# Optimization experiments

Hardware: AMD Instinct MI355X
Metric: run time of the kernel (lower is better)

Reference implementation:

```python
import jax, jax.numpy as jnp
import numpy as np

N = 100000   # nodes
E = 1600000  # edges
IN = 32      # input_dim == num_concepts
H = 128      # h_dim == num_concepts * dim_per_concept
C = 32       # num_concepts
D = 4        # dim_per_concept
G = 32       # g_dim of per-concept MLPs
LAMBDAV = 1e-3


def _spmm(edge_src, edge_dst, edge_val, x):
    # sparse adjacency matmul: out[d] = sum_{edges e: dst(e)=d} val(e) * x[src(e)]
    return jax.ops.segment_sum(edge_val[:, None] * x[edge_src], edge_dst, num_segments=N)


def setup_inputs() -> dict:
    key = jax.random.key(0)
    ks = jax.random.split(key, 20)
    s = lambda shape: 1.0 / np.sqrt(shape[-1] if len(shape) > 1 else 1)
    inp = {
        'X': jax.random.normal(ks[0], (N, IN), jnp.float32),
        'label': jax.random.uniform(ks[1], (N, C), jnp.float32),
        'edge_val': jax.random.uniform(ks[2], (E,), jnp.float32),
        'noise': jax.random.normal(ks[3], (N, C, D), jnp.float32),
        'W_base': jax.random.normal(ks[4], (IN, H), jnp.float32) / np.sqrt(IN),
        'W_mean': jax.random.normal(ks[5], (H, H), jnp.float32) / np.sqrt(H),
        'W_logstd': jax.random.normal(ks[6], (H, H), jnp.float32) / np.sqrt(H),
        'A': 0.05 * jax.random.normal(ks[7], (C, C), jnp.float32),  # keep I - A^T well-conditioned
        'Wz1': jax.random.normal(ks[8], (C, D, G), jnp.float32) / np.sqrt(D),
        'bz1': jax.random.normal(ks[9], (C, G), jnp.float32) * 0.01,
        'Wz2': jax.random.normal(ks[10], (C, G, D), jnp.float32) / np.sqrt(G),
        'bz2': jax.random.normal(ks[11], (C, D), jnp.float32) * 0.01,
        'Wl1': jax.random.normal(ks[12], (C, 1, G), jnp.float32),
        'bl1': jax.random.normal(ks[13], (C, G), jnp.float32) * 0.01,
        'Wl2': jax.random.normal(ks[14], (C, G, 1), jnp.float32) / np.sqrt(G),
        'bl2': jax.random.normal(ks[15], (C, 1), jnp.float32) * 0.01,
        'Wrec': jax.random.normal(ks[16], (H, IN), jnp.float32) / np.sqrt(H),
        'brec': jax.random.normal(ks[17], (IN,), jnp.float32) * 0.01,
        'edge_src': jax.random.randint(ks[18], (E,), 0, N),
        'edge_dst': jax.random.randint(ks[19], (E,), 0, N),
    }
    return inp


def reference(X, label, edge_val, noise, W_base, W_mean, W_logstd, A,
              Wz1, bz1, Wz2, bz2, Wl1, bl1, Wl2, bl2, Wrec, brec,
              edge_src, edge_dst):
    # ---- sparse GCN encoder (x branch): GraphConvSparse = act(spmm(adj, x @ W)) ----
    hidden = jax.nn.relu(_spmm(edge_src, edge_dst, edge_val, X @ W_base))   # [N, H]
    e_m = _spmm(edge_src, edge_dst, edge_val, hidden @ W_mean)              # [N, H]
    _ = _spmm(edge_src, edge_dst, edge_val, hidden @ W_logstd)              # computed then discarded (e_v := ones) in source
    e_m = e_m.reshape(N, C, D)                                              # [N, C, D]

    # ---- CausalDAG: z = (I - A^T)^{-1} epsilon along the concept axis ----
    I = jnp.eye(C, dtype=X.dtype)
    Cmat = jnp.linalg.inv(I - A.T)                                          # [C, C]
    z_m = jnp.einsum('ck,nkd->ncd', Cmat, e_m)                              # [N, C, D]

    # mask: A^T @ x along concept axis
    masked_z_m = jnp.einsum('ck,nkd->ncd', A.T, z_m)                        # [N, C, D]
    masked_label = jnp.einsum('ck,nk->nc', A.T, label)[..., None]           # [N, C, 1]

    # g_z: per-concept MLP Linear(D,G)-ELU-Linear(G,D), weights stacked over concepts
    hz = jax.nn.elu(jnp.einsum('ncd,cdg->ncg', masked_z_m, Wz1) + bz1[None])
    masked_z_m = jnp.einsum('ncg,cgd->ncd', hz, Wz2) + bz2[None]            # [N, C, D]

    # g_label: per-concept MLP Linear(1,G)-ELU-Linear(G,1)
    hl = jax.nn.elu(jnp.einsum('nce,ceg->ncg', masked_label, Wl1) + bl1[None])
    pred_label = (jnp.einsum('ncg,cge->nce', hl, Wl2) + bl2[None])[..., 0]  # [N, C]

    # conditional_sample_gaussian with v = e_v * lambdav, e_v = ones
    z = masked_z_m + jnp.sqrt(jnp.asarray(LAMBDAV, X.dtype)) * noise        # [N, C, D]

    # pred_x / reconst_X head
    rec_x = z.reshape(N, H) @ Wrec + brec                                   # [N, IN]
    return rec_x, pred_label
```

## Files before the change

kernel.cpp:

```cpp
#include <hip/hip_runtime.h>
#include <hip/hip_bf16.h>

#define N_NODES 100000
#define N_EDGES 1600000
#define NBUCK   391
#define EHIST_G 196

static __device__ __forceinline__ float us2f(unsigned short u) {
    union { unsigned int i; float f; } cv; cv.i = ((unsigned int)u) << 16; return cv.f;
}
static __device__ __forceinline__ unsigned short f2us(float f) {
    __hip_bfloat16 b = __float2bfloat16(f);
    union { __hip_bfloat16 b; unsigned short u; } cv; cv.b = b; return cv.u;
}
static __device__ __forceinline__ float elu_fast(float v) {
    return v > 0.f ? v : (__expf(v) - 1.0f);
}

__global__ __launch_bounds__(64) void k_inv(const float* __restrict__ A,
                                            float* __restrict__ MmT) {
    __shared__ float Af[1024];
    __shared__ float aug[32 * 65];
    __shared__ float fac[32];
    __shared__ float pv_s;
    int t = threadIdx.x;
    for (int i = t; i < 1024; i += 64) Af[i] = A[i];
    __syncthreads();
    for (int i = t; i < 2048; i += 64) {
        int r = i >> 6, c = i & 63;
        float v;
        if (c < 32) v = (r == c ? 1.0f : 0.0f) - Af[c * 32 + r];
        else        v = ((c - 32) == r ? 1.0f : 0.0f);
        aug[r * 65 + c] = v;
    }
    __syncthreads();
    for (int k = 0; k < 32; ++k) {
        if (t == 0) pv_s = 1.0f / aug[k * 65 + k];
        __syncthreads();
        aug[k * 65 + t] *= pv_s;
        __syncthreads();
        if (t < 32) fac[t] = aug[t * 65 + k];
        __syncthreads();
        #pragma unroll 4
        for (int i = t; i < 2048; i += 64) {
            int r = i >> 6, c = i & 63;
            if (r != k) aug[r * 65 + c] -= fac[r] * aug[k * 65 + c];
        }
        __syncthreads();
    }
    for (int i = t; i < 1024; i += 64) {
        int j = i >> 5, c = i & 31;
        float s = 0.f;
        #pragma unroll
        for (int k = 0; k < 32; ++k) s += Af[k * 32 + c] * aug[k * 65 + 32 + j];
        MmT[i] = s;
    }
}

__global__ __launch_bounds__(256) void k_fold(const float* __restrict__ MmT,
                                              const float* __restrict__ Wm,
                                              float* __restrict__ Wcomb) {
    __shared__ float MmTs[1024];
    int tid = threadIdx.x;
    for (int i = tid; i < 1024; i += 256) MmTs[i] = MmT[i];
    __syncthreads();
    int o = blockIdx.x * 256 + tid;
    int h = o >> 5, c = o & 31;
    float4 s = {0.f, 0.f, 0.f, 0.f};
    #pragma unroll
    for (int j = 0; j < 32; ++j) {
        float m = MmTs[j * 32 + c];
        float4 w = ((const float4*)Wm)[h * 32 + j];
        s.x += m * w.x; s.y += m * w.y; s.z += m * w.z; s.w += m * w.w;
    }
    ((float4*)Wcomb)[o] = s;
}

__global__ __launch_bounds__(256) void k_bhist(const int* __restrict__ edst,
                                               unsigned int* __restrict__ bucket_deg) {
    __shared__ unsigned int h[NBUCK];
    int tid = threadIdx.x;
    int e0 = blockIdx.x * 8192;
    for (int i = tid; i < NBUCK; i += 256) h[i] = 0u;
    __syncthreads();
    #pragma unroll 4
    for (int k = 0; k < 32; ++k) {
        int e = e0 + k * 256 + tid;
        if (e < N_EDGES) atomicAdd(&h[((unsigned)edst[e]) >> 8], 1u);
    }
    __syncthreads();
    for (int b = tid; b < NBUCK; b += 256) {
        unsigned int v = h[b];
        if (v) atomicAdd(&bucket_deg[b], v);
    }
}

__global__ __launch_bounds__(512) void k_bscan(const unsigned int* __restrict__ bucket_deg,
                                               unsigned int* __restrict__ bucket_start,
                                               unsigned int* __restrict__ bucket_cursor) {
    __shared__ unsigned int s[512];
    int tid = threadIdx.x;
    unsigned int v = (tid < NBUCK) ? bucket_deg[tid] : 0u;
    s[tid] = v;
    __syncthreads();
    for (int off = 1; off < 512; off <<= 1) {
        unsigned int x = (tid >= off) ? s[tid - off] : 0u;
        __syncthreads();
        s[tid] += x;
        __syncthreads();
    }
    if (tid < NBUCK) {
        unsigned int excl = s[tid] - v;
        bucket_start[tid] = excl;
        bucket_cursor[tid] = excl;
    }
    if (tid == 0) bucket_start[NBUCK] = N_EDGES;
}

__global__ __launch_bounds__(256) void k_bucket1(const int* __restrict__ esrc,
                                                 const int* __restrict__ edst,
                                                 const float* __restrict__ evalv,
                                                 unsigned int* __restrict__ bucket_cursor,
                                                 uint2* __restrict__ coarse,
                                                 unsigned char* __restrict__ coarse_dl) {
    __shared__ unsigned int hist[NBUCK];
    __shared__ unsigned int gbase[NBUCK];
    __shared__ unsigned int lcnt[NBUCK];
    int tid = threadIdx.x;
    int e0 = blockIdx.x * 8192;
    for (int i = tid; i < NBUCK; i += 256) { hist[i] = 0u; lcnt[i] = 0u; }
    __syncthreads();
    #pragma unroll 4
    for (int k = 0; k < 32; ++k) {
        int e = e0 + k * 256 + tid;
        if (e < N_EDGES) atomicAdd(&hist[((unsigned)edst[e]) >> 8], 1u);
    }
    __syncthreads();
    for (int b = tid; b < NBUCK; b += 256) {
        unsigned int h = hist[b];
        gbase[b] = h ? atomicAdd(&bucket_cursor[b], h) : 0u;
    }
    __syncthreads();
    #pragma unroll 4
    for (int k = 0; k < 32; ++k) {
        int e = e0 + k * 256 + tid;
        if (e < N_EDGES) {
            unsigned int d = (unsigned)edst[e];
            unsigned int b = d >> 8;
            unsigned int r = atomicAdd(&lcnt[b], 1u);
            unsigned int p = gbase[b] + r;
            uint2 ev;
            ev.x = (unsigned int)esrc[e];
            ev.y = __float_as_uint(evalv[e]);
            coarse[p] = ev;
            coarse_dl[p] = (unsigned char)(d & 255u);
        }
    }
}

__global__ __launch_bounds__(256) void k_bucket2(const unsigned int* __restrict__ bucket_start,
                                                 const uint2* __restrict__ coarse,
                                                 const unsigned char* __restrict__ coarse_dl,
                                                 unsigned int* __restrict__ row_start,
                                                 uint2* __restrict__ edge_sorted) {
    __shared__ unsigned int h[256];
    __shared__ unsigned int sc[256];
    int b = blockIdx.x;
    int tid = threadIdx.x;
    unsigned int bs = bucket_start[b];
    unsigned int be = bucket_start[b + 1];
    h[tid] = 0u;
    __syncthreads();
    for (unsigned int i = bs + tid; i < be; i += 256)
        atomicAdd(&h[coarse_dl[i]], 1u);
    __syncthreads();
    unsigned int v = h[tid];
    sc[tid] = v;
    __syncthreads();
    for (int off = 1; off < 256; off <<= 1) {
        unsigned int x = (tid >= off) ? sc[tid - off] : 0u;
        __syncthreads();
        sc[tid] += x;
        __syncthreads();
    }
    unsigned int excl = sc[tid] - v;
    int node = (b << 8) + tid;
    if (node < N_NODES) row_start[node] = bs + excl;
    if (b == 0 && tid == 0) row_start[N_NODES] = N_EDGES;
    h[tid] = excl;
    __syncthreads();
    for (unsigned int i = bs + tid; i < be; i += 256) {
        uint2 ev = coarse[i];
        unsigned int dl = coarse_dl[i];
        unsigned int r = atomicAdd(&h[dl], 1u);
        edge_sorted[bs + r] = ev;
    }
}

__global__ __launch_bounds__(256) void k_fuse1(const unsigned int* __restrict__ row_start,
                                               const uint2* __restrict__ edge_sorted,
                                               const float* __restrict__ X,
                                               const float* __restrict__ Wb,
                                               unsigned short* __restrict__ hidden) {
    __shared__ float Wb_s[4096];
    __shared__ float s1r[8 * 33];
    int tid = threadIdx.x;
    for (int i = tid; i < 1024; i += 256)
        ((float4*)Wb_s)[i] = ((const float4*)Wb)[i];

    int lane = tid & 31;
    int nd = tid >> 5;
    int n = blockIdx.x * 8 + nd;
    unsigned int i = row_start[n], e = row_start[n + 1];
    float a0 = 0.f, a1 = 0.f, a2 = 0.f, a3 = 0.f;
    for (; i + 4 <= e; i += 4) {
        uint2 ea = edge_sorted[i + 0], eb = edge_sorted[i + 1];
        uint2 ec = edge_sorted[i + 2], ed = edge_sorted[i + 3];
        float xa = X[(size_t)ea.x * 32 + lane];
        float xb = X[(size_t)eb.x * 32 + lane];
        float xc = X[(size_t)ec.x * 32 + lane];
        float xd = X[(size_t)ed.x * 32 + lane];
        a0 += __uint_as_float(ea.y) * xa;
        a1 += __uint_as_float(eb.y) * xb;
        a2 += __uint_as_float(ec.y) * xc;
        a3 += __uint_as_float(ed.y) * xd;
    }
    for (; i < e; ++i) {
        uint2 ea = edge_sorted[i];
        a0 += __uint_as_float(ea.y) * X[(size_t)ea.x * 32 + lane];
    }
    s1r[nd * 33 + lane] = (a0 + a1) + (a2 + a3);
    __syncthreads();

    int q = lane * 4;
    float4 acc = {0.f, 0.f, 0.f, 0.f};
    #pragma unroll
    for (int k = 0; k < 32; ++k) {
        float v = s1r[nd * 33 + k];
        float4 w = *(const float4*)&Wb_s[k * 128 + q];
        acc.x += v * w.x; acc.y += v * w.y; acc.z += v * w.z; acc.w += v * w.w;
    }
    ushort4 o;
    o.x = f2us(fmaxf(acc.x, 0.f)); o.y = f2us(fmaxf(acc.y, 0.f));
    o.z = f2us(fmaxf(acc.z, 0.f)); o.w = f2us(fmaxf(acc.w, 0.f));
    *(ushort4*)&hidden[(size_t)n * 128 + q] = o;
}

__global__ __launch_bounds__(256) void k_gather2(const unsigned int* __restrict__ row_start,
                                                 const uint2* __restrict__ edge_sorted,
                                                 const unsigned short* __restrict__ hidden,
                                                 unsigned short* __restrict__ S2) {
    int lane = threadIdx.x & 31;
    int n = blockIdx.x * 8 + (threadIdx.x >> 5);
    unsigned int i = row_start[n], e = row_start[n + 1];
    float4 A0 = {0, 0, 0, 0}, A1 = {0, 0, 0, 0}, A2 = {0, 0, 0, 0}, A3 = {0, 0, 0, 0};
    for (; i + 4 <= e; i += 4) {
        uint2 ea = edge_sorted[i + 0], eb = edge_sorted[i + 1];
        uint2 ec = edge_sorted[i + 2], ed = edge_sorted[i + 3];
        ushort4 ha = *(const ushort4*)&hidden[(size_t)ea.x * 128 + lane * 4];
        ushort4 hb = *(const ushort4*)&hidden[(size_t)eb.x * 128 + lane * 4];
        ushort4 hc = *(const ushort4*)&hidden[(size_t)ec.x * 128 + lane * 4];
        ushort4 hd = *(const ushort4*)&hidden[(size_t)ed.x * 128 + lane * 4];
        float va = __uint_as_float(ea.y), vb = __uint_as_float(eb.y);
        float vc = __uint_as_float(ec.y), vd = __uint_as_float(ed.y);
        A0.x += va * us2f(ha.x); A0.y += va * us2f(ha.y); A0.z += va * us2f(ha.z); A0.w += va * us2f(ha.w);
        A1.x += vb * us2f(hb.x); A1.y += vb * us2f(hb.y); A1.z += vb * us2f(hb.z); A1.w += vb * us2f(hb.w);
        A2.x += vc * us2f(hc.x); A2.y += vc * us2f(hc.y); A2.z += vc * us2f(hc.z); A2.w += vc * us2f(hc.w);
        A3.x += vd * us2f(hd.x); A3.y += vd * us2f(hd.y); A3.z += vd * us2f(hd.z); A3.w += vd * us2f(hd.w);
    }
    for (; i < e; ++i) {
        uint2 ea = edge_sorted[i];
        float v = __uint_as_float(ea.y);
        ushort4 h = *(const ushort4*)&hidden[(size_t)ea.x * 128 + lane * 4];
        A0.x += v * us2f(h.x); A0.y += v * us2f(h.y); A0.z += v * us2f(h.z); A0.w += v * us2f(h.w);
    }
    float4 acc;
    acc.x = (A0.x + A1.x) + (A2.x + A3.x);
    acc.y = (A0.y + A1.y) + (A2.y + A3.y);
    acc.z = (A0.z + A1.z) + (A2.z + A3.z);
    acc.w = (A0.w + A1.w) + (A2.w + A3.w);
    ushort4 o;
    o.x = f2us(acc.x); o.y = f2us(acc.y); o.z = f2us(acc.z); o.w = f2us(acc.w);
    *(ushort4*)&S2[(size_t)n * 128 + lane * 4] = o;
}

__global__ __launch_bounds__(256) void k_gemm2(const unsigned short* __restrict__ S2,
                                               const float* __restrict__ Wc,
                                               unsigned short* __restrict__ mt4) {
    __shared__ float Wc_s[128 * 64];
    __shared__ float S2s[32 * 132];
    __shared__ unsigned short Tt[64 * 40];
    int tid = threadIdx.x;
    int rb = blockIdx.x >> 1;
    int j0 = (blockIdx.x & 1) * 64;
    int n0 = rb * 32;
    for (int idx = tid; idx < 2048; idx += 256) {
        int k = idx >> 4, jq = idx & 15;
        *(float4*)&Wc_s[k * 64 + jq * 4] = *(const float4*)&Wc[k * 128 + j0 + jq * 4];
    }
    for (int idx = tid; idx < 1024; idx += 256) {
        int r = idx >> 5, kq = idx & 31;
        ushort4 h = *(const ushort4*)&S2[(size_t)(n0 + r) * 128 + kq * 4];
        float4 f = {us2f(h.x), us2f(h.y), us2f(h.z), us2f(h.w)};
        *(float4*)&S2s[r * 132 + kq * 4] = f;
    }
    __syncthreads();
    int q = (tid & 15) * 4;
    int r0 = tid >> 4;
    float4 a0 = {0, 0, 0, 0}, a1 = {0, 0, 0, 0};
    for (int k4 = 0; k4 < 128; k4 += 4) {
        float4 s0 = *(const float4*)&S2s[r0 * 132 + k4];
        float4 s1 = *(const float4*)&S2s[(r0 + 16) * 132 + k4];
        #pragma unroll
        for (int kk = 0; kk < 4; ++kk) {
            float v0 = (&s0.x)[kk];
            float v1 = (&s1.x)[kk];
            float4 w = *(const float4*)&Wc_s[(k4 + kk) * 64 + q];
            a0.x += v0 * w.x; a0.y += v0 * w.y; a0.z += v0 * w.z; a0.w += v0 * w.w;
            a1.x += v1 * w.x; a1.y += v1 * w.y; a1.z += v1 * w.z; a1.w += v1 * w.w;
        }
    }
    #pragma unroll
    for (int c = 0; c < 4; ++c) {
        Tt[(q + c) * 40 + r0]      = f2us((&a0.x)[c]);
        Tt[(q + c) * 40 + r0 + 16] = f2us((&a1.x)[c]);
    }
    __syncthreads();
    int cc = tid >> 4;
    int r  = (tid & 15) * 2;
    int cg = (j0 >> 2) + cc;
    #pragma unroll
    for (int rr = 0; rr < 2; ++rr) {
        ushort4 o;
        o.x = Tt[(cc * 4 + 0) * 40 + r + rr];
        o.y = Tt[(cc * 4 + 1) * 40 + r + rr];
        o.z = Tt[(cc * 4 + 2) * 40 + r + rr];
        o.w = Tt[(cc * 4 + 3) * 40 + r + rr];
        *(ushort4*)&mt4[((size_t)cg * N_NODES + n0 + r + rr) * 4] = o;
    }
}

__global__ __launch_bounds__(256) void k_noisew(const float* __restrict__ noise,
                                                const float* __restrict__ Wrec,
                                                const float* __restrict__ brec,
                                                float* __restrict__ noiseW) {
    __shared__ float Wr[4096];
    __shared__ float Ns[64 * 132];
    __shared__ float brs[32];
    int tid = threadIdx.x;
    int n0 = blockIdx.x * 64;
    const float SQ = 0.03162277660168379f;
    for (int i = tid; i < 1024; i += 256)
        ((float4*)Wr)[i] = ((const float4*)Wrec)[i];
    if (tid < 32) brs[tid] = brec[tid];
    for (int i = tid; i < 1024; i += 256) {
        int row = i >> 4, u8 = i & 15;
        int n = n0 + row;
        float4 f0, f1;
        if (n < N_NODES) {
            f0 = ((const float4*)(noise + (size_t)n * 128))[u8 * 2];
            f1 = ((const float4*)(noise + (size_t)n * 128))[u8 * 2 + 1];
        } else {
            f0 = make_float4(0.f, 0.f, 0.f, 0.f);
            f1 = f0;
        }
        *(float4*)&Ns[row * 132 + u8 * 8]     = make_float4(SQ * f0.x, SQ * f0.y, SQ * f0.z, SQ * f0.w);
        *(float4*)&Ns[row * 132 + u8 * 8 + 4] = make_float4(SQ * f1.x, SQ * f1.y, SQ * f1.z, SQ * f1.w);
    }
    __syncthreads();
    int r = tid >> 2, q = (tid & 3) * 8;
    float4 acc0 = {0, 0, 0, 0}, acc1 = {0, 0, 0, 0};
    for (int k = 0; k < 128; ++k) {
        float nv = Ns[r * 132 + k];
        float4 w0 = *(const float4*)&Wr[k * 32 + q];
        float4 w1 = *(const float4*)&Wr[k * 32 + q + 4];
        acc0.x += nv * w0.x; acc0.y += nv * w0.y; acc0.z += nv * w0.z; acc0.w += nv * w0.w;
        acc1.x += nv * w1.x; acc1.y += nv * w1.y; acc1.z += nv * w1.z; acc1.w += nv * w1.w;
    }
    int n = n0 + r;
    if (n < N_NODES) {
        acc0.x += brs[q];     acc0.y += brs[q + 1]; acc0.z += brs[q + 2]; acc0.w += brs[q + 3];
        acc1.x += brs[q + 4]; acc1.y += brs[q + 5]; acc1.z += brs[q + 6]; acc1.w += brs[q + 7];
        ((float4*)(noiseW + (size_t)n * 32 + q))[0] = acc0;
        ((float4*)(noiseW + (size_t)n * 32 + q + 4))[0] = acc1;
    }
}

__global__ __launch_bounds__(512) void k_nodez(const unsigned short* __restrict__ mt4,
                                               const float* __restrict__ Wz1,
                                               const float* __restrict__ bz1,
                                               const float* __restrict__ Wz2,
                                               const float* __restrict__ bz2,
                                               const float* __restrict__ Wrec,
                                               const float* __restrict__ noiseW,
                                               float* __restrict__ out) {
    __shared__ float scr[3 * 128 * 34];
    int tid = threadIdx.x;
    int lt  = tid & 127;
    int qq  = tid >> 7;
    int c0  = __builtin_amdgcn_readfirstlane(qq * 8);
    int n = blockIdx.x * 128 + lt;
    bool ok = n < N_NODES;
    int m = ok ? n : (N_NODES - 1);

    const float4* W1 = (const float4*)Wz1;
    const float4* B1 = (const float4*)bz1;
    const float4* W2 = (const float4*)Wz2;
    const float4* B2 = (const float4*)bz2;
    const float4* WR = (const float4*)Wrec;

    float4 o0 = {0,0,0,0}, o1 = {0,0,0,0}, o2 = {0,0,0,0}, o3 = {0,0,0,0};
    float4 o4v = {0,0,0,0}, o5 = {0,0,0,0}, o6 = {0,0,0,0}, o7 = {0,0,0,0};

    ushort4 mz = *(const ushort4*)&mt4[((size_t)c0 * N_NODES + m) * 4];

    for (int cc = 0; cc < 8; ++cc) {
        int c = c0 + cc;
        int cn = (cc < 7) ? (c + 1) : c;
        ushort4 nmz = *(const ushort4*)&mt4[((size_t)cn * N_NODES + m) * 4];
        float a0 = us2f(mz.x), a1 = us2f(mz.y), a2 = us2f(mz.z), a3 = us2f(mz.w);

        float4 zb = B2[c];
        float4 z = zb;
        #pragma unroll
        for (int g4 = 0; g4 < 8; ++g4) {
            float4 w0 = W1[c * 32 + g4];
            float4 w1 = W1[c * 32 + 8 + g4];
            float4 w2 = W1[c * 32 + 16 + g4];
            float4 w3 = W1[c * 32 + 24 + g4];
            float4 bb = B1[c * 8 + g4];
            float4 v;
            v.x = bb.x + a0 * w0.x + a1 * w1.x + a2 * w2.x + a3 * w3.x;
            v.y = bb.y + a0 * w0.y + a1 * w1.y + a2 * w2.y + a3 * w3.y;
            v.z = bb.z + a0 * w0.z + a1 * w1.z + a2 * w2.z + a3 * w3.z;
            v.w = bb.w + a0 * w0.w + a1 * w1.w + a2 * w2.w + a3 * w3.w;
            v.x = elu_fast(v.x); v.y = elu_fast(v.y); v.z = elu_fast(v.z); v.w = elu_fast(v.w);
            float4 u0 = W2[c * 32 + g4 * 4 + 0];
            float4 u1 = W2[c * 32 + g4 * 4 + 1];
            float4 u2 = W2[c * 32 + g4 * 4 + 2];
            float4 u3 = W2[c * 32 + g4 * 4 + 3];
            z.x += v.x * u0.x + v.y * u1.x + v.z * u2.x + v.w * u3.x;
            z.y += v.x * u0.y + v.y * u1.y + v.z * u2.y + v.w * u3.y;
            z.z += v.x * u0.z + v.y * u1.z + v.z * u2.z + v.w * u3.z;
            z.w += v.x * u0.w + v.y * u1.w + v.z * u2.w + v.w * u3.w;
        }
        #pragma unroll
        for (int d = 0; d < 4; ++d) {
            float zv = (&z.x)[d];
            const float4* wr = &WR[(c * 4 + d) * 8];
            float4 r0 = wr[0], r1 = wr[1], r2 = wr[2], r3 = wr[3];
            float4 r4 = wr[4], r5 = wr[5], r6 = wr[6], r7 = wr[7];
            o0.x += zv * r0.x; o0.y += zv * r0.y; o0.z += zv * r0.z; o0.w += zv * r0.w;
            o1.x += zv * r1.x; o1.y += zv * r1.y; o1.z += zv * r1.z; o1.w += zv * r1.w;
            o2.x += zv * r2.x; o2.y += zv * r2.y; o2.z += zv * r2.z; o2.w += zv * r2.w;
            o3.x += zv * r3.x; o3.y += zv * r3.y; o3.z += zv * r3.z; o3.w += zv * r3.w;
            o4v.x += zv * r4.x; o4v.y += zv * r4.y; o4v.z += zv * r4.z; o4v.w += zv * r4.w;
            o5.x += zv * r5.x; o5.y += zv * r5.y; o5.z += zv * r5.z; o5.w += zv * r5.w;
            o6.x += zv * r6.x; o6.y += zv * r6.y; o6.z += zv * r6.z; o6.w += zv * r6.w;
            o7.x += zv * r7.x; o7.y += zv * r7.y; o7.z += zv * r7.z; o7.w += zv * r7.w;
        }
        mz = nmz;
    }

    __syncthreads();
    if (qq != 0) {
        float* p = &scr[((qq - 1) * 128 + lt) * 34];
        *(float2*)&p[0]  = make_float2(o0.x, o0.y);  *(float2*)&p[2]  = make_float2(o0.z, o0.w);
        *(float2*)&p[4]  = make_float2(o1.x, o1.y);  *(float2*)&p[6]  = make_float2(o1.z, o1.w);
        *(float2*)&p[8]  = make_float2(o2.x, o2.y);  *(float2*)&p[10] = make_float2(o2.z, o2.w);
        *(float2*)&p[12] = make_float2(o3.x, o3.y);  *(float2*)&p[14] = make_float2(o3.z, o3.w);
        *(float2*)&p[16] = make_float2(o4v.x, o4v.y); *(float2*)&p[18] = make_float2(o4v.z, o4v.w);
        *(float2*)&p[20] = make_float2(o5.x, o5.y);  *(float2*)&p[22] = make_float2(o5.z, o5.w);
        *(float2*)&p[24] = make_float2(o6.x, o6.y);  *(float2*)&p[26] = make_float2(o6.z, o6.w);
        *(float2*)&p[28] = make_float2(o7.x, o7.y);  *(float2*)&p[30] = make_float2(o7.z, o7.w);
    }
    __syncthreads();
    if (qq == 0 && ok) {
        const float* pA = &scr[lt * 34];
        const float* pB = &scr[(128 + lt) * 34];
        const float* pC = &scr[(256 + lt) * 34];
        const float4* nw = (const float4*)(noiseW + (size_t)n * 32);
        float4* po = (float4*)(out + (size_t)n * 32);
        float4 w, t;
        w = nw[0];
        t.x = o0.x + pA[0] + pB[0] + pC[0] + w.x;   t.y = o0.y + pA[1] + pB[1] + pC[1] + w.y;
        t.z = o0.z + pA[2] + pB[2] + pC[2] + w.z;   t.w = o0.w + pA[3] + pB[3] + pC[3] + w.w;
        po[0] = t;
        w = nw[1];
        t.x = o1.x + pA[4] + pB[4] + pC[4] + w.x;   t.y = o1.y + pA[5] + pB[5] + pC[5] + w.y;
        t.z = o1.z + pA[6] + pB[6] + pC[6] + w.z;   t.w = o1.w + pA[7] + pB[7] + pC[7] + w.w;
        po[1] = t;
        w = nw[2];
        t.x = o2.x + pA[8] + pB[8] + pC[8] + w.x;   t.y = o2.y + pA[9] + pB[9] + pC[9] + w.y;
        t.z = o2.z + pA[10] + pB[10] + pC[10] + w.z; t.w = o2.w + pA[11] + pB[11] + pC[11] + w.w;
        po[2] = t;
        w = nw[3];
        t.x = o3.x + pA[12] + pB[12] + pC[12] + w.x; t.y = o3.y + pA[13] + pB[13] + pC[13] + w.y;
        t.z = o3.z + pA[14] + pB[14] + pC[14] + w.z; t.w = o3.w + pA[15] + pB[15] + pC[15] + w.w;
        po[3] = t;
        w = nw[4];
        t.x = o4v.x + pA[16] + pB[16] + pC[16] + w.x; t.y = o4v.y + pA[17] + pB[17] + pC[17] + w.y;
        t.z = o4v.z + pA[18] + pB[18] + pC[18] + w.z; t.w = o4v.w + pA[19] + pB[19] + pC[19] + w.w;
        po[4] = t;
        w = nw[5];
        t.x = o5.x + pA[20] + pB[20] + pC[20] + w.x; t.y = o5.y + pA[21] + pB[21] + pC[21] + w.y;
        t.z = o5.z + pA[22] + pB[22] + pC[22] + w.z; t.w = o5.w + pA[23] + pB[23] + pC[23] + w.w;
        po[5] = t;
        w = nw[6];
        t.x = o6.x + pA[24] + pB[24] + pC[24] + w.x; t.y = o6.y + pA[25] + pB[25] + pC[25] + w.y;
        t.z = o6.z + pA[26] + pB[26] + pC[26] + w.z; t.w = o6.w + pA[27] + pB[27] + pC[27] + w.w;
        po[6] = t;
        w = nw[7];
        t.x = o7.x + pA[28] + pB[28] + pC[28] + w.x; t.y = o7.y + pA[29] + pB[29] + pC[29] + w.y;
        t.z = o7.z + pA[30] + pB[30] + pC[30] + w.z; t.w = o7.w + pA[31] + pB[31] + pC[31] + w.w;
        po[7] = t;
    }
}

__global__ __launch_bounds__(256) void k_label(const float* __restrict__ label,
                                               const float* __restrict__ A,
                                               const float* __restrict__ Wl1,
                                               const float* __restrict__ bl1,
                                               const float* __restrict__ Wl2,
                                               const float* __restrict__ bl2,
                                               float* __restrict__ out) {
    __shared__ float As[1024], Wl1s[1024], bl1s[1024], Wl2s[1024], bl2s[32];
    int tid = threadIdx.x;
    for (int i = tid; i < 1024; i += 256) {
        As[i] = A[i];
        Wl1s[i] = Wl1[i];
        bl1s[i] = bl1[i];
        Wl2s[i] = Wl2[i];
    }
    if (tid < 32) bl2s[tid] = bl2[tid];
    __syncthreads();

    int n = blockIdx.x * 256 + tid;
    bool ok = n < N_NODES;
    int nn = ok ? n : (N_NODES - 1);

    float lab[32];
    #pragma unroll
    for (int q = 0; q < 8; ++q) {
        float4 lv = ((const float4*)(label + (size_t)nn * 32))[q];
        lab[q * 4 + 0] = lv.x; lab[q * 4 + 1] = lv.y;
        lab[q * 4 + 2] = lv.z; lab[q * 4 + 3] = lv.w;
    }
    float pred[32];
    for (int c = 0; c < 32; ++c) {
        float ml = 0.f;
        #pragma unroll
        for (int k = 0; k < 32; ++k) ml += As[k * 32 + c] * lab[k];
        float p = bl2s[c];
        #pragma unroll
        for (int g = 0; g < 32; ++g) {
            float h = elu_fast(ml * Wl1s[c * 32 + g] + bl1s[c * 32 + g]);
            p += h * Wl2s[c * 32 + g];
        }
        pred[c] = p;
    }
    if (ok) {
        #pragma unroll
        for (int q = 0; q < 8; ++q) {
            float4 v = {pred[q * 4 + 0], pred[q * 4 + 1], pred[q * 4 + 2], pred[q * 4 + 3]};
            ((float4*)(out + (size_t)N_NODES * 32 + (size_t)n * 32))[q] = v;
        }
    }
}

extern "C" void kernel_launch(void* const* d_in, const int* in_sizes, int n_in,
                              void* d_out, int out_size, void* d_ws, size_t ws_size,
                              hipStream_t stream) {
    const float* X      = (const float*)d_in[0];
    const float* label  = (const float*)d_in[1];
    const float* evalv  = (const float*)d_in[2];
    const float* noise  = (const float*)d_in[3];
    const float* W_base = (const float*)d_in[4];
    const float* W_mean = (const float*)d_in[5];
    const float* A      = (const float*)d_in[7];
    const float* Wz1    = (const float*)d_in[8];
    const float* bz1    = (const float*)d_in[9];
    const float* Wz2    = (const float*)d_in[10];
    const float* bz2    = (const float*)d_in[11];
    const float* Wl1    = (const float*)d_in[12];
    const float* bl1    = (const float*)d_in[13];
    const float* Wl2    = (const float*)d_in[14];
    const float* bl2    = (const float*)d_in[15];
    const float* Wrec   = (const float*)d_in[16];
    const float* brec   = (const float*)d_in[17];
    const int* esrc = (const int*)d_in[18];
    const int* edst = (const int*)d_in[19];
    float* out = (float*)d_out;

    char* ws = (char*)d_ws;
    float*          Wcomb        = (float*)(ws);
    float*          MmT          = (float*)(ws + 65536);
    unsigned int*   bucket_deg   = (unsigned int*)(ws + 69632);
    unsigned int*   bucket_start = (unsigned int*)(ws + 71680);
    unsigned int*   bucket_cursor= (unsigned int*)(ws + 73728);
    unsigned int*   row_start    = (unsigned int*)(ws + 472064);
    uint2*          edge_sorted  = (uint2*)(ws + 1273984);
    uint2*          coarse       = (uint2*)(ws + 14073984);
    unsigned char*  coarse_dl    = (unsigned char*)(ws + 26873984);
    unsigned short* hidden       = (unsigned short*)(ws + 14073984);
    unsigned short* mt4          = (unsigned short*)(ws + 14073984);
    unsigned short* S2           = (unsigned short*)(ws + 39673984);
    float*          noiseW       = (float*)(ws + 39673984);

    hipMemsetAsync(bucket_deg, 0, 2048, stream);
    k_inv<<<1, 64, 0, stream>>>(A, MmT);
    k_fold<<<16, 256, 0, stream>>>(MmT, W_mean, Wcomb);
    k_bhist<<<EHIST_G, 256, 0, stream>>>(edst, bucket_deg);
    k_bscan<<<1, 512, 0, stream>>>(bucket_deg, bucket_start, bucket_cursor);
    k_bucket1<<<EHIST_G, 256, 0, stream>>>(esrc, edst, evalv,
                                           bucket_cursor, coarse, coarse_dl);
    k_bucket2<<<NBUCK, 256, 0, stream>>>(bucket_start, coarse, coarse_dl,
                                         row_start, edge_sorted);
    k_fuse1<<<N_NODES / 8, 256, 0, stream>>>(row_start, edge_sorted, X, W_base, hidden);
    k_gather2<<<N_NODES / 8, 256, 0, stream>>>(row_start, edge_sorted, hidden, S2);
    k_gemm2<<<(N_NODES / 32) * 2, 256, 0, stream>>>(S2, Wcomb, mt4);
    k_noisew<<<(N_NODES + 63) / 64, 256, 0, stream>>>(noise, Wrec, brec, noiseW);
    k_nodez<<<(N_NODES + 127) / 128, 512, 0, stream>>>(mt4,
                                                       Wz1, bz1, Wz2, bz2,
                                                       Wrec, noiseW, out);
    k_label<<<(N_NODES + 255) / 256, 256, 0, stream>>>(label, A, Wl1, bl1, Wl2, bl2, out);
}
```

Baseline: 679.3 us.

## Merge inverse and fold kernels, reuse per-block histograms, gather X in bf16

Fuses the matrix-inverse and weight-fold kernels into one 1024-thread block, which removes a launch and a global round trip. The per-block bucket histograms are now written to global memory and reused by the bucket pass, so the second histogram pass and the memset go away. X is converted to bf16 once, halving the bytes fetched by the first sparse gather, at the cost of an extra conversion kernel and reduced input precision.

Measured after the change: 624.4 us. 1.09x faster.

```diff
diff --git a/kernel.cpp b/kernel.cpp
--- a/kernel.cpp
+++ b/kernel.cpp
@@ -17,16 +17,18 @@
     return v > 0.f ? v : (__expf(v) - 1.0f);
 }
 
-__global__ __launch_bounds__(64) void k_inv(const float* __restrict__ A,
-                                            float* __restrict__ MmT) {
+__global__ __launch_bounds__(1024) void k_prep(const float* __restrict__ A,
+                                               const float* __restrict__ Wm,
+                                               float* __restrict__ Wcomb) {
     __shared__ float Af[1024];
     __shared__ float aug[32 * 65];
+    __shared__ float MmTs[1024];
     __shared__ float fac[32];
     __shared__ float pv_s;
     int t = threadIdx.x;
-    for (int i = t; i < 1024; i += 64) Af[i] = A[i];
-    __syncthreads();
-    for (int i = t; i < 2048; i += 64) {
+    Af[t] = A[t];
+    __syncthreads();
+    for (int i = t; i < 2048; i += 1024) {
         int r = i >> 6, c = i & 63;
         float v;
         if (c < 32) v = (r == c ? 1.0f : 0.0f) - Af[c * 32 + r];
@@ -37,47 +39,48 @@
     for (int k = 0; k < 32; ++k) {
         if (t == 0) pv_s = 1.0f / aug[k * 65 + k];
         __syncthreads();
-        aug[k * 65 + t] *= pv_s;
+        if (t < 64) aug[k * 65 + t] *= pv_s;
         __syncthreads();
         if (t < 32) fac[t] = aug[t * 65 + k];
         __syncthreads();
-        #pragma unroll 4
-        for (int i = t; i < 2048; i += 64) {
+        for (int i = t; i < 2048; i += 1024) {
             int r = i >> 6, c = i & 63;
             if (r != k) aug[r * 65 + c] -= fac[r] * aug[k * 65 + c];
         }
         __syncthreads();
     }
-    for (int i = t; i < 1024; i += 64) {
-        int j = i >> 5, c = i & 31;
+    {
+        int j = t >> 5, c = t & 31;
         float s = 0.f;
         #pragma unroll
         for (int k = 0; k < 32; ++k) s += Af[k * 32 + c] * aug[k * 65 + 32 + j];
-        MmT[i] = s;
-    }
-}
-
-__global__ __launch_bounds__(256) void k_fold(const float* __restrict__ MmT,
-                                              const float* __restrict__ Wm,
-                                              float* __restrict__ Wcomb) {
-    __shared__ float MmTs[1024];
-    int tid = threadIdx.x;
-    for (int i = tid; i < 1024; i += 256) MmTs[i] = MmT[i];
-    __syncthreads();
-    int o = blockIdx.x * 256 + tid;
-    int h = o >> 5, c = o & 31;
-    float4 s = {0.f, 0.f, 0.f, 0.f};
-    #pragma unroll
-    for (int j = 0; j < 32; ++j) {
-        float m = MmTs[j * 32 + c];
-        float4 w = ((const float4*)Wm)[h * 32 + j];
-        s.x += m * w.x; s.y += m * w.y; s.z += m * w.z; s.w += m * w.w;
-    }
-    ((float4*)Wcomb)[o] = s;
+        MmTs[t] = s;
+    }
+    __syncthreads();
+    for (int o = t; o < 4096; o += 1024) {
+        int h = o >> 5, c = o & 31;
+        float4 s = {0.f, 0.f, 0.f, 0.f};
+        #pragma unroll
+        for (int j = 0; j < 32; ++j) {
+            float m = MmTs[j * 32 + c];
+            float4 w = ((const float4*)Wm)[h * 32 + j];
+            s.x += m * w.x; s.y += m * w.y; s.z += m * w.z; s.w += m * w.w;
+        }
+        ((float4*)Wcomb)[o] = s;
+    }
+}
+
+__global__ __launch_bounds__(256) void k_x16(const float* __restrict__ X,
+                                             unsigned short* __restrict__ Xh) {
+    int i = blockIdx.x * 256 + threadIdx.x;
+    float4 v = ((const float4*)X)[i];
+    ushort4 o;
+    o.x = f2us(v.x); o.y = f2us(v.y); o.z = f2us(v.z); o.w = f2us(v.w);
+    ((ushort4*)Xh)[i] = o;
 }
 
 __global__ __launch_bounds__(256) void k_bhist(const int* __restrict__ edst,
-                                               unsigned int* __restrict__ bucket_deg) {
+                                               unsigned int* __restrict__ blk_hist) {
     __shared__ unsigned int h[NBUCK];
     int tid = threadIdx.x;
     int e0 = blockIdx.x * 8192;
@@ -89,18 +92,20 @@
         if (e < N_EDGES) atomicAdd(&h[((unsigned)edst[e]) >> 8], 1u);
     }
     __syncthreads();
-    for (int b = tid; b < NBUCK; b += 256) {
-        unsigned int v = h[b];
-        if (v) atomicAdd(&bucket_deg[b], v);
-    }
-}
-
-__global__ __launch_bounds__(512) void k_bscan(const unsigned int* __restrict__ bucket_deg,
+    for (int b = tid; b < NBUCK; b += 256)
+        blk_hist[(size_t)blockIdx.x * NBUCK + b] = h[b];
+}
+
+__global__ __launch_bounds__(512) void k_bscan(const unsigned int* __restrict__ blk_hist,
                                                unsigned int* __restrict__ bucket_start,
                                                unsigned int* __restrict__ bucket_cursor) {
     __shared__ unsigned int s[512];
     int tid = threadIdx.x;
-    unsigned int v = (tid < NBUCK) ? bucket_deg[tid] : 0u;
+    unsigned int v = 0u;
+    if (tid < NBUCK) {
+        for (int g = 0; g < EHIST_G; ++g)
+            v += blk_hist[(size_t)g * NBUCK + tid];
+    }
     s[tid] = v;
     __syncthreads();
     for (int off = 1; off < 512; off <<= 1) {
@@ -120,25 +125,18 @@
 __global__ __launch_bounds__(256) void k_bucket1(const int* __restrict__ esrc,
                                                  const int* __restrict__ edst,
                                                  const float* __restrict__ evalv,
+                                                 const unsigned int* __restrict__ blk_hist,
                                                  unsigned int* __restrict__ bucket_cursor,
                                                  uint2* __restrict__ coarse,
                                                  unsigned char* __restrict__ coarse_dl) {
-    __shared__ unsigned int hist[NBUCK];
     __shared__ unsigned int gbase[NBUCK];
     __shared__ unsigned int lcnt[NBUCK];
     int tid = threadIdx.x;
     int e0 = blockIdx.x * 8192;
-    for (int i = tid; i < NBUCK; i += 256) { hist[i] = 0u; lcnt[i] = 0u; }
-    __syncthreads();
-    #pragma unroll 4
-    for (int k = 0; k < 32; ++k) {
-        int e = e0 + k * 256 + tid;
-        if (e < N_EDGES) atomicAdd(&hist[((unsigned)edst[e]) >> 8], 1u);
-    }
-    __syncthreads();
     for (int b = tid; b < NBUCK; b += 256) {
-        unsigned int h = hist[b];
+        unsigned int h = blk_hist[(size_t)blockIdx.x * NBUCK + b];
         gbase[b] = h ? atomicAdd(&bucket_cursor[b], h) : 0u;
+        lcnt[b] = 0u;
     }
     __syncthreads();
     #pragma unroll 4
@@ -199,7 +197,7 @@
 
 __global__ __launch_bounds__(256) void k_fuse1(const unsigned int* __restrict__ row_start,
                                                const uint2* __restrict__ edge_sorted,
-                                               const float* __restrict__ X,
+                                               const unsigned short* __restrict__ Xh,
                                                const float* __restrict__ Wb,
                                                unsigned short* __restrict__ hidden) {
     __shared__ float Wb_s[4096];
@@ -216,10 +214,10 @@
     for (; i + 4 <= e; i += 4) {
         uint2 ea = edge_sorted[i + 0], eb = edge_sorted[i + 1];
         uint2 ec = edge_sorted[i + 2], ed = edge_sorted[i + 3];
-        float xa = X[(size_t)ea.x * 32 + lane];
-        float xb = X[(size_t)eb.x * 32 + lane];
-        float xc = X[(size_t)ec.x * 32 + lane];
-        float xd = X[(size_t)ed.x * 32 + lane];
+        float xa = us2f(Xh[(size_t)ea.x * 32 + lane]);
+        float xb = us2f(Xh[(size_t)eb.x * 32 + lane]);
+        float xc = us2f(Xh[(size_t)ec.x * 32 + lane]);
+        float xd = us2f(Xh[(size_t)ed.x * 32 + lane]);
         a0 += __uint_as_float(ea.y) * xa;
         a1 += __uint_as_float(eb.y) * xb;
         a2 += __uint_as_float(ec.y) * xc;
@@ -227,7 +225,7 @@
     }
     for (; i < e; ++i) {
         uint2 ea = edge_sorted[i];
-        a0 += __uint_as_float(ea.y) * X[(size_t)ea.x * 32 + lane];
+        a0 += __uint_as_float(ea.y) * us2f(Xh[(size_t)ea.x * 32 + lane]);
     }
     s1r[nd * 33 + lane] = (a0 + a1) + (a2 + a3);
     __syncthreads();
@@ -594,10 +592,9 @@
 
     char* ws = (char*)d_ws;
     float*          Wcomb        = (float*)(ws);
-    float*          MmT          = (float*)(ws + 65536);
-    unsigned int*   bucket_deg   = (unsigned int*)(ws + 69632);
     unsigned int*   bucket_start = (unsigned int*)(ws + 71680);
     unsigned int*   bucket_cursor= (unsigned int*)(ws + 73728);
+    unsigned int*   blk_hist     = (unsigned int*)(ws + 76800);
     unsigned int*   row_start    = (unsigned int*)(ws + 472064);
     uint2*          edge_sorted  = (uint2*)(ws + 1273984);
     uint2*          coarse       = (uint2*)(ws + 14073984);
@@ -606,17 +603,17 @@
     unsigned short* mt4          = (unsigned short*)(ws + 14073984);
     unsigned short* S2           = (unsigned short*)(ws + 39673984);
     float*          noiseW       = (float*)(ws + 39673984);
-
-    hipMemsetAsync(bucket_deg, 0, 2048, stream);
-    k_inv<<<1, 64, 0, stream>>>(A, MmT);
-    k_fold<<<16, 256, 0, stream>>>(MmT, W_mean, Wcomb);
-    k_bhist<<<EHIST_G, 256, 0, stream>>>(edst, bucket_deg);
-    k_bscan<<<1, 512, 0, stream>>>(bucket_deg, bucket_start, bucket_cursor);
-    k_bucket1<<<EHIST_G, 256, 0, stream>>>(esrc, edst, evalv,
+    unsigned short* Xh           = (unsigned short*)(ws + 65273984);
+
+    k_prep<<<1, 1024, 0, stream>>>(A, W_mean, Wcomb);
+    k_x16<<<800000 / 256, 256, 0, stream>>>(X, Xh);
+    k_bhist<<<EHIST_G, 256, 0, stream>>>(edst, blk_hist);
+    k_bscan<<<1, 512, 0, stream>>>(blk_hist, bucket_start, bucket_cursor);
+    k_bucket1<<<EHIST_G, 256, 0, stream>>>(esrc, edst, evalv, blk_hist,
                                            bucket_cursor, coarse, coarse_dl);
     k_bucket2<<<NBUCK, 256, 0, stream>>>(bucket_start, coarse, coarse_dl,
                                          row_start, edge_sorted);
-    k_fuse1<<<N_NODES / 8, 256, 0, stream>>>(row_start, edge_sorted, X, W_base, hidden);
+    k_fuse1<<<N_NODES / 8, 256, 0, stream>>>(row_start, edge_sorted, Xh, W_base, hidden);
     k_gather2<<<N_NODES / 8, 256, 0, stream>>>(row_start, edge_sorted, hidden, S2);
     k_gemm2<<<(N_NODES / 32) * 2, 256, 0, stream>>>(S2, Wcomb, mt4);
     k_noisew<<<(N_NODES + 63) / 64, 256, 0, stream>>>(noise, Wrec, brec, noiseW);
```
